# Performance work log

Hardware: AMD Instinct MI355X
Metric: run time of the kernel (lower is better)

## Reference

```python
import jax, jax.numpy as jnp
import numpy as np

N, D, H, E, TOP_K = 8192, 1024, 4096, 8, 2


def setup_inputs() -> dict:
    key = jax.random.key(0)
    ks = jax.random.split(key, 6)
    input_batch = jax.random.normal(ks[0], (N, D), dtype=jnp.float32)
    # Router-style top-k: distinct expert ids per token, softmax-normalized weights
    logits = jax.random.normal(ks[1], (N, E), dtype=jnp.float32)
    topk_vals, indices = jax.lax.top_k(logits, TOP_K)          # [N, k]
    probabilities = jax.nn.softmax(topk_vals, axis=-1)          # [N, k]
    scale1 = 1.0 / np.sqrt(D)
    scale2 = 1.0 / np.sqrt(H)
    W1 = jax.random.normal(ks[2], (E, D, H), dtype=jnp.float32) * scale1
    b1 = jnp.zeros((E, H), dtype=jnp.float32)
    W2 = jax.random.normal(ks[3], (E, H, D), dtype=jnp.float32) * scale2
    b2 = jnp.zeros((E, D), dtype=jnp.float32)
    return {
        "input_batch": input_batch,
        "probabilities": probabilities,
        "indices": indices.astype(jnp.int64),
        "W1": W1, "b1": b1, "W2": W2, "b2": b2,
    }


def reference(input_batch, probabilities, indices, W1, b1, W2, b2):
    # Each expert is Linear(D->H) + ReLU + Linear(H->D).
    # Dense per-expert forward (batched GEMM over the expert axis), then
    # gather the top_k selected expert outputs per token and combine with
    # router probabilities applied AFTER the experts:
    #   out[n] = sum_k p[n,k] * expert_{idx[n,k]}(x[n])
    h = jax.nn.relu(jnp.einsum("nd,edh->enh", input_batch, W1) + b1[:, None, :])
    y = jnp.einsum("enh,eho->eno", h, W2) + b2[:, None, :]      # [E, N, D]
    y_tok = jnp.swapaxes(y, 0, 1)                                # [N, E, D]
    sel = jnp.take_along_axis(y_tok, indices[:, :, None], axis=1)  # [N, k, D]
    output = jnp.sum(probabilities[:, :, None] * sel, axis=1)    # [N, D]
    total_loss = jnp.asarray(0.0, dtype=input_batch.dtype)       # sampler+expert losses are zero here
    return output, total_loss
```

## Files before the change

kernel.cpp:

```cpp
#include <hip/hip_runtime.h>
#include <hip/hip_bf16.h>

#define N_TOK 8192
#define DDIM 1024
#define HDIM 4096
#define NEXP 8
#define TOPK 2
#define NK (N_TOK*TOPK)
#define BM 128
#define BK 32
#define MAXT 136

typedef __hip_bfloat16 bf16;
typedef __attribute__((ext_vector_type(8))) short bf16x8;
typedef __attribute__((ext_vector_type(4))) float f32x4;

__device__ __forceinline__ void gload16(const void* g, void* lds) {
  auto l = (__attribute__((address_space(3))) unsigned int*)(unsigned int)(unsigned long long)lds;
  auto gg = (const __attribute__((address_space(1))) unsigned int*)(unsigned long long)g;
  __builtin_amdgcn_global_load_lds(gg, l, 16, 0, 0);
}

__global__ void k_router(const int* __restrict__ idx, int stride,
                         int* __restrict__ offp, int* __restrict__ texp,
                         int* __restrict__ tok, int* __restrict__ pos) {
  __shared__ int cnt[NEXP], so[NEXP + 1], off2[NEXP], scnt[NEXP];
  int tid = threadIdx.x;
  if (tid < NEXP) cnt[tid] = 0;
  __syncthreads();
  for (int r = tid; r < NK; r += blockDim.x) {
    int e = idx[r * stride];
    e = min(max(e, 0), NEXP - 1);
    atomicAdd(&cnt[e], 1);
  }
  __syncthreads();
  if (tid == 0) {
    int cum = 0;
    for (int e = 0; e < NEXP; e++) {
      so[e] = cum;
      cum += ((cnt[e] + BM - 1) / BM) * BM;
    }
    so[NEXP] = cum;
    for (int e = 0; e <= NEXP; e++) offp[e] = so[e];
  }
  __syncthreads();
  if (tid < NEXP) { off2[tid] = so[tid]; scnt[tid] = cnt[tid]; }
  __syncthreads();
  for (int r = tid; r < NK; r += blockDim.x) {
    int e = idx[r * stride];
    e = min(max(e, 0), NEXP - 1);
    int p = atomicAdd(&off2[e], 1);
    tok[p] = r >> 1;
    pos[r] = p;
  }
  int total_tiles = so[NEXP] / BM;
  for (int t = tid; t < MAXT; t += blockDim.x) {
    int e = -1;
    if (t < total_tiles) {
      for (int q = 0; q < NEXP; q++)
        if (t * BM >= so[q] && t * BM < so[q + 1]) e = q;
    }
    texp[t] = e;
  }
  for (int e = 0; e < NEXP; e++) {
    int start = so[e] + scnt[e], end = so[e + 1];
    for (int i = start + tid; i < end; i += blockDim.x) tok[i] = 0;
  }
}

__global__ void k_cvt_x(const float* __restrict__ x, bf16* __restrict__ xb) {
  int i = blockIdx.x * blockDim.x + threadIdx.x;
  if (i >= N_TOK * DDIM / 8) return;
  float4 a = ((const float4*)x)[(size_t)i * 2];
  float4 b = ((const float4*)x)[(size_t)i * 2 + 1];
  union { bf16 h[8]; uint4 v; } u;
  u.h[0] = __float2bfloat16(a.x); u.h[1] = __float2bfloat16(a.y);
  u.h[2] = __float2bfloat16(a.z); u.h[3] = __float2bfloat16(a.w);
  u.h[4] = __float2bfloat16(b.x); u.h[5] = __float2bfloat16(b.y);
  u.h[6] = __float2bfloat16(b.z); u.h[7] = __float2bfloat16(b.w);
  *(uint4*)&xb[(size_t)i * 8] = u.v;
}

__global__ void k_transpose(const float* __restrict__ in, bf16* __restrict__ out,
                            int R, int C) {
  __shared__ float t[32][65];
  size_t ebase = (size_t)blockIdx.z * R * C;
  int r0 = blockIdx.y * 32, c0 = blockIdx.x * 64;
  int tid = threadIdx.x;
  {
    int lr = tid >> 3, lc = (tid & 7) * 8;
    const float4* src = (const float4*)&in[ebase + (size_t)(r0 + lr) * C + c0 + lc];
    float4 a = src[0], b = src[1];
    t[lr][lc + 0] = a.x; t[lr][lc + 1] = a.y; t[lr][lc + 2] = a.z; t[lr][lc + 3] = a.w;
    t[lr][lc + 4] = b.x; t[lr][lc + 5] = b.y; t[lr][lc + 6] = b.z; t[lr][lc + 7] = b.w;
  }
  __syncthreads();
  {
    int sc = tid >> 2, sr = (tid & 3) * 8;
    union { bf16 h[8]; uint4 v; } u;
#pragma unroll
    for (int j = 0; j < 8; j++) u.h[j] = __float2bfloat16(t[sr + j][sc]);
    *(uint4*)&out[ebase + (size_t)(c0 + sc) * R + r0 + sr] = u.v;
  }
}

template<int MODE>
__global__ __launch_bounds__(512, 4) void k_gemm(
    const bf16* __restrict__ A, const bf16* __restrict__ Bt,
    const float* __restrict__ bias, const int* __restrict__ texp,
    const int* __restrict__ tok, int tile_base, void* __restrict__ Cout)
{
  constexpr int KT   = MODE ? HDIM : DDIM;
  constexpr int NCOL = MODE ? DDIM : HDIM;
  constexpr int BN   = 256;
  constexpr int GX   = NCOL / BN;
  constexpr int NT   = KT / BK;
  constexpr int BUFB = (BM + BN) * BK * 2;

  int nwg = gridDim.x, orig = blockIdx.x;
  int q8 = nwg >> 3, r8 = nwg & 7;
  int xcd = orig & 7, jj0 = orig >> 3;
  int w = (xcd < r8 ? xcd * (q8 + 1) : r8 * (q8 + 1) + (xcd - r8) * q8) + jj0;
  int tn = w % GX;
  int tmr = w / GX;
  int tm = tile_base + tmr;
  int e = texp[tm];
  if (e < 0) return;

  int tid = threadIdx.x, lane = tid & 63, wid = tid >> 6;
  int wm = wid >> 2, wn = wid & 3;
  int lr = lane & 15, kg = lane >> 4;

  __shared__ __align__(16) char lds[3 * BUFB];

  unsigned goff[3];
  {
    int row = tid >> 2, c = tid & 3;
    int ch = c ^ ((row >> 1) & 3);
    int arow = MODE ? (tmr * BM + row) : tok[tm * BM + row];
    goff[0] = (unsigned)(arow * KT + ch * 8);
    goff[1] = (unsigned)((e * NCOL + tn * BN + row) * KT + ch * 8);
    goff[2] = (unsigned)((e * NCOL + tn * BN + 128 + row) * KT + ch * 8);
  }

  auto stage = [&](int kt, int buf) {
    char* base = lds + buf * BUFB;
    gload16(A + goff[0] + kt * BK, base + tid * 16);
    gload16(Bt + goff[1] + kt * BK, base + 8192 + tid * 16);
    gload16(Bt + goff[2] + kt * BK, base + 16384 + tid * 16);
  };

  f32x4 acc[4][4];
#pragma unroll
  for (int i = 0; i < 4; i++)
#pragma unroll
    for (int j = 0; j < 4; j++) acc[i][j] = (f32x4){0.f, 0.f, 0.f, 0.f};

  stage(0, 0);
  stage(1, 1);
  asm volatile("s_waitcnt vmcnt(3)" ::: "memory");
  __builtin_amdgcn_s_barrier();

#pragma unroll 1
  for (int kt = 0; kt < NT; ++kt) {
    if (kt + 2 < NT) stage(kt + 2, (kt + 2) % 3);

    const char* base = lds + (kt % 3) * BUFB;
    bf16x8 av[4], bv[4];
#pragma unroll
    for (int mi = 0; mi < 4; ++mi) {
      int m = wm * 64 + mi * 16 + lr;
      int slot = kg ^ ((m >> 1) & 3);
      av[mi] = *(const bf16x8*)(base + m * 64 + slot * 16);
    }
#pragma unroll
    for (int ni = 0; ni < 4; ++ni) {
      int n = wn * 64 + ni * 16 + lr;
      int slot = kg ^ ((n >> 1) & 3);
      bv[ni] = *(const bf16x8*)(base + 8192 + n * 64 + slot * 16);
    }

#pragma unroll
    for (int mi = 0; mi < 4; ++mi)
#pragma unroll
      for (int ni = 0; ni < 4; ++ni)
        acc[mi][ni] = __builtin_amdgcn_mfma_f32_16x16x32_bf16(
            av[mi], bv[ni], acc[mi][ni], 0, 0, 0);

    if (kt + 1 < NT) {
      if (kt + 2 < NT) asm volatile("s_waitcnt vmcnt(3)" ::: "memory");
      else             asm volatile("s_waitcnt vmcnt(0)" ::: "memory");
      __builtin_amdgcn_s_barrier();
    }
  }

  const float* be = bias + (size_t)e * NCOL;
  int crow0 = (MODE ? tm : tmr) * BM;
#pragma unroll
  for (int ni = 0; ni < 4; ++ni) {
    int n = tn * BN + wn * 64 + ni * 16 + lr;
    float bvv = be[n];
#pragma unroll
    for (int mi = 0; mi < 4; ++mi) {
#pragma unroll
      for (int j = 0; j < 4; j++) {
        int mrow = wm * 64 + mi * 16 + kg * 4 + j;
        float v = acc[mi][ni][j] + bvv;
        if (MODE == 0) v = fmaxf(v, 0.f);
        ((bf16*)Cout)[(size_t)(crow0 + mrow) * NCOL + n] = __float2bfloat16(v);
      }
    }
  }
}

__global__ void k_combine(const bf16* __restrict__ y, const float* __restrict__ prob,
                          const int* __restrict__ pos, float* __restrict__ out) {
  int gid = blockIdx.x * blockDim.x + threadIdx.x;
  if (gid >= N_TOK * DDIM / 8) return;
  int n = gid >> 7;
  int d8 = gid & 127;
  int r0 = pos[2 * n], r1 = pos[2 * n + 1];
  float p0 = prob[2 * n], p1 = prob[2 * n + 1];
  uint4 a = *(const uint4*)&y[(size_t)r0 * DDIM + d8 * 8];
  uint4 b = *(const uint4*)&y[(size_t)r1 * DDIM + d8 * 8];
  const unsigned short* ah = (const unsigned short*)&a;
  const unsigned short* bh = (const unsigned short*)&b;
  float o[8];
#pragma unroll
  for (int k = 0; k < 8; k++) {
    float fa = __uint_as_float((unsigned)ah[k] << 16);
    float fb = __uint_as_float((unsigned)bh[k] << 16);
    o[k] = p0 * fa + p1 * fb;
  }
  float4* op = (float4*)&out[(size_t)n * DDIM + d8 * 8];
  op[0] = (float4){o[0], o[1], o[2], o[3]};
  op[1] = (float4){o[4], o[5], o[6], o[7]};
  if (gid == 0) out[(size_t)N_TOK * DDIM] = 0.f;
}

extern "C" void kernel_launch(void* const* d_in, const int* in_sizes, int n_in,
                              void* d_out, int out_size, void* d_ws, size_t ws_size,
                              hipStream_t stream) {
  const float* x    = (const float*)d_in[0];
  const float* prob = (const float*)d_in[1];
  const int*   idx  = (const int*)d_in[2];
  const float* W1   = (const float*)d_in[3];
  const float* b1   = (const float*)d_in[4];
  const float* W2   = (const float*)d_in[5];
  const float* b2   = (const float*)d_in[6];
  float* out = (float*)d_out;
  int stride = (in_sizes[2] == NK) ? 1 : 2;

  char* ws = (char*)d_ws;
  size_t cur = 0;
  auto alloc = [&](size_t bytes) -> void* {
    cur = (cur + 255) & ~(size_t)255;
    void* p = ws + cur; cur += bytes; return p;
  };
  int* offp  = (int*)alloc((NEXP + 1) * 4);
  int* texp  = (int*)alloc(MAXT * 4);
  int* tok   = (int*)alloc((size_t)MAXT * BM * 4);
  int* pos   = (int*)alloc((size_t)NK * 4);
  bf16* Xb   = (bf16*)alloc((size_t)N_TOK * DDIM * 2);
  bf16* W1t  = (bf16*)alloc((size_t)NEXP * HDIM * DDIM * 2);
  bf16* W2t  = (bf16*)alloc((size_t)NEXP * DDIM * HDIM * 2);
  bf16* ybuf = (bf16*)alloc((size_t)MAXT * BM * DDIM * 2);
  cur = (cur + 255) & ~(size_t)255;
  size_t h_off = cur;
  size_t h_avail = ws_size > h_off ? ws_size - h_off : 0;
  long long ts_ll = (long long)(h_avail / ((size_t)BM * HDIM * 2));
  int ts = (int)(ts_ll < 1 ? 1 : (ts_ll > MAXT ? MAXT : ts_ll));
  bf16* hbuf = (bf16*)(ws + h_off);

  k_router<<<1, 1024, 0, stream>>>(idx, stride, offp, texp, tok, pos);
  k_cvt_x<<<(N_TOK * DDIM / 8 + 255) / 256, 256, 0, stream>>>(x, Xb);
  k_transpose<<<dim3(HDIM / 64, DDIM / 32, NEXP), 256, 0, stream>>>(W1, W1t, DDIM, HDIM);
  k_transpose<<<dim3(DDIM / 64, HDIM / 32, NEXP), 256, 0, stream>>>(W2, W2t, HDIM, DDIM);

  for (int base = 0; base < MAXT; base += ts) {
    int cnt_t = (MAXT - base < ts) ? (MAXT - base) : ts;
    k_gemm<0><<<dim3(cnt_t * (HDIM / 256)), 512, 0, stream>>>(
        Xb, W1t, b1, texp, tok, base, (void*)hbuf);
    k_gemm<1><<<dim3(cnt_t * (DDIM / 256)), 512, 0, stream>>>(
        hbuf, W2t, b2, texp, tok, base, (void*)ybuf);
  }
  k_combine<<<(N_TOK * DDIM / 8 + 255) / 256, 256, 0, stream>>>(ybuf, prob, pos, out);
}
```

Measured before the change: 471.0 us.

## Enlarge GEMM tiles to 256x256x64 with 8-phase ping-pong LDS schedule

Increases the expert GEMM tile from 128x256 to 256x256 rows and the K step from 32 to 64. The main loop is restructured into an 8-phase double-buffered schedule that interleaves LDS reads, global-to-LDS loads and MFMA quarters, separated by barriers, and uses s_setprio to favour MFMA issue. The aim is higher arithmetic intensity per byte loaded and better overlap of memory with compute. The cost is lower occupancy (2 blocks per CU, 128KB LDS), more padding waste per expert tile, and a higher register footprint.

```diff
diff --git a/kernel.cpp b/kernel.cpp
--- a/kernel.cpp
+++ b/kernel.cpp
@@ -7,9 +7,9 @@
 #define NEXP 8
 #define TOPK 2
 #define NK (N_TOK*TOPK)
-#define BM 128
-#define BK 32
-#define MAXT 136
+#define BM 256
+#define BK 64
+#define MAXT 72
 
 typedef __hip_bfloat16 bf16;
 typedef __attribute__((ext_vector_type(8))) short bf16x8;
@@ -105,17 +105,17 @@
 }
 
 template<int MODE>
-__global__ __launch_bounds__(512, 4) void k_gemm(
+__global__ __launch_bounds__(512, 2) void k_gemm(
     const bf16* __restrict__ A, const bf16* __restrict__ Bt,
     const float* __restrict__ bias, const int* __restrict__ texp,
     const int* __restrict__ tok, int tile_base, void* __restrict__ Cout)
 {
-  constexpr int KT   = MODE ? HDIM : DDIM;
-  constexpr int NCOL = MODE ? DDIM : HDIM;
-  constexpr int BN   = 256;
-  constexpr int GX   = NCOL / BN;
-  constexpr int NT   = KT / BK;
-  constexpr int BUFB = (BM + BN) * BK * 2;
+  constexpr int KT    = MODE ? HDIM : DDIM;
+  constexpr int NCOL  = MODE ? DDIM : HDIM;
+  constexpr int GX    = NCOL / 256;
+  constexpr int NT    = KT / BK;
+  constexpr int NITER = NT / 2;
+  constexpr int BUFB  = 65536;
 
   int nwg = gridDim.x, orig = blockIdx.x;
   int q8 = nwg >> 3, r8 = nwg & 7;
@@ -131,86 +131,142 @@
   int wm = wid >> 2, wn = wid & 3;
   int lr = lane & 15, kg = lane >> 4;
 
-  __shared__ __align__(16) char lds[3 * BUFB];
-
-  unsigned goff[3];
-  {
-    int row = tid >> 2, c = tid & 3;
-    int ch = c ^ ((row >> 1) & 3);
-    int arow = MODE ? (tmr * BM + row) : tok[tm * BM + row];
-    goff[0] = (unsigned)(arow * KT + ch * 8);
-    goff[1] = (unsigned)((e * NCOL + tn * BN + row) * KT + ch * 8);
-    goff[2] = (unsigned)((e * NCOL + tn * BN + 128 + row) * KT + ch * 8);
-  }
-
-  auto stage = [&](int kt, int buf) {
-    char* base = lds + buf * BUFB;
-    gload16(A + goff[0] + kt * BK, base + tid * 16);
-    gload16(Bt + goff[1] + kt * BK, base + 8192 + tid * 16);
-    gload16(Bt + goff[2] + kt * BK, base + 16384 + tid * 16);
-  };
-
-  f32x4 acc[4][4];
-#pragma unroll
-  for (int i = 0; i < 4; i++)
+  __shared__ __align__(16) char lds[2 * BUFB];
+
+  unsigned aoff[2][2], boff[2][2];
+#pragma unroll
+  for (int h = 0; h < 2; ++h) {
+#pragma unroll
+    for (int it = 0; it < 2; ++it) {
+      int idx = it * 512 + tid, rl = idx >> 3, c = idx & 7;
+      int ch = c ^ (rl & 7);
+      int arow = MODE ? (tmr * BM + h * 128 + rl) : tok[tm * BM + h * 128 + rl];
+      aoff[h][it] = (unsigned)(arow * KT + ch * 8);
+      boff[h][it] = (unsigned)((e * NCOL + tn * 256 + h * 128 + rl) * KT + ch * 8);
+    }
+  }
+
+  auto stA = [&](int kt, int h) {
+    char* dst = lds + (kt & 1) * BUFB + h * 16384;
+    gload16(A + (size_t)aoff[h][0] + kt * BK, dst + tid * 16);
+    gload16(A + (size_t)aoff[h][1] + kt * BK, dst + 8192 + tid * 16);
+  };
+  auto stB = [&](int kt, int h) {
+    char* dst = lds + (kt & 1) * BUFB + 32768 + h * 16384;
+    gload16(Bt + (size_t)boff[h][0] + kt * BK, dst + tid * 16);
+    gload16(Bt + (size_t)boff[h][1] + kt * BK, dst + 8192 + tid * 16);
+  };
+
+  f32x4 acc[8][4];
+#pragma unroll
+  for (int i = 0; i < 8; i++)
 #pragma unroll
     for (int j = 0; j < 4; j++) acc[i][j] = (f32x4){0.f, 0.f, 0.f, 0.f};
 
-  stage(0, 0);
-  stage(1, 1);
-  asm volatile("s_waitcnt vmcnt(3)" ::: "memory");
-  __builtin_amdgcn_s_barrier();
+  bf16x8 bv[8];
+  auto readB8 = [&](const char* buf) {
+    const char* bb = buf + 32768;
+#pragma unroll
+    for (int ni = 0; ni < 4; ++ni)
+#pragma unroll
+      for (int kh = 0; kh < 2; ++kh) {
+        int r = wn * 64 + ni * 16 + lr;
+        int ck = (kh * 4 + kg) ^ (r & 7);
+        bv[ni * 2 + kh] = *(const bf16x8*)(bb + r * 128 + ck * 16);
+      }
+  };
+  auto readA4 = [&](const char* buf, int q, bf16x8* av) {
+#pragma unroll
+    for (int g = 0; g < 2; ++g)
+#pragma unroll
+      for (int kh = 0; kh < 2; ++kh) {
+        int r = wm * 128 + (q * 2 + g) * 16 + lr;
+        int ck = (kh * 4 + kg) ^ (r & 7);
+        av[g * 2 + kh] = *(const bf16x8*)(buf + r * 128 + ck * 16);
+      }
+  };
+  auto mfmaQ = [&](int q, bf16x8* av) {
+    __builtin_amdgcn_s_setprio(1);
+#pragma unroll
+    for (int g = 0; g < 2; ++g)
+#pragma unroll
+      for (int ni = 0; ni < 4; ++ni)
+#pragma unroll
+        for (int kh = 0; kh < 2; ++kh)
+          acc[q * 2 + g][ni] = __builtin_amdgcn_mfma_f32_16x16x32_bf16(
+              av[g * 2 + kh], bv[ni * 2 + kh], acc[q * 2 + g][ni], 0, 0, 0);
+    __builtin_amdgcn_s_setprio(0);
+  };
+
+#define BAR()    __builtin_amdgcn_s_barrier()
+#define LGKM0()  asm volatile("s_waitcnt lgkmcnt(0)" ::: "memory")
+#define LGKM8()  asm volatile("s_waitcnt lgkmcnt(8)" ::: "memory")
+
+  stA(0, 0); stA(0, 1); stB(0, 0); stB(0, 1);
+  stB(1, 0); stB(1, 1);
+  asm volatile("s_waitcnt vmcnt(4)" ::: "memory");
+  BAR();
+
+  const char* b0 = lds;
+  const char* b1 = lds + BUFB;
 
 #pragma unroll 1
-  for (int kt = 0; kt < NT; ++kt) {
-    if (kt + 2 < NT) stage(kt + 2, (kt + 2) % 3);
-
-    const char* base = lds + (kt % 3) * BUFB;
-    bf16x8 av[4], bv[4];
-#pragma unroll
-    for (int mi = 0; mi < 4; ++mi) {
-      int m = wm * 64 + mi * 16 + lr;
-      int slot = kg ^ ((m >> 1) & 3);
-      av[mi] = *(const bf16x8*)(base + m * 64 + slot * 16);
-    }
-#pragma unroll
-    for (int ni = 0; ni < 4; ++ni) {
-      int n = wn * 64 + ni * 16 + lr;
-      int slot = kg ^ ((n >> 1) & 3);
-      bv[ni] = *(const bf16x8*)(base + 8192 + n * 64 + slot * 16);
-    }
-
-#pragma unroll
-    for (int mi = 0; mi < 4; ++mi)
-#pragma unroll
-      for (int ni = 0; ni < 4; ++ni)
-        acc[mi][ni] = __builtin_amdgcn_mfma_f32_16x16x32_bf16(
-            av[mi], bv[ni], acc[mi][ni], 0, 0, 0);
-
-    if (kt + 1 < NT) {
-      if (kt + 2 < NT) asm volatile("s_waitcnt vmcnt(3)" ::: "memory");
-      else             asm volatile("s_waitcnt vmcnt(0)" ::: "memory");
-      __builtin_amdgcn_s_barrier();
-    }
+  for (int i = 0; i < NITER; ++i) {
+    int t = 2 * i;
+    bool last = (i == NITER - 1);
+    bf16x8 av[4];
+
+    readB8(b0); readA4(b0, 0, av);
+    stA(t + 1, 0);
+    LGKM8();
+    BAR(); LGKM0(); mfmaQ(0, av); BAR();
+
+    readA4(b0, 1, av); stA(t + 1, 1);
+    BAR(); LGKM0(); mfmaQ(1, av); BAR();
+
+    readA4(b0, 2, av); if (!last) stB(t + 2, 0);
+    BAR(); LGKM0(); mfmaQ(2, av); BAR();
+
+    readA4(b0, 3, av); if (!last) stB(t + 2, 1);
+    if (last) { asm volatile("s_waitcnt vmcnt(0)" ::: "memory"); }
+    else      { asm volatile("s_waitcnt vmcnt(4)" ::: "memory"); }
+    BAR(); LGKM0(); mfmaQ(3, av); BAR();
+
+    readB8(b1); readA4(b1, 0, av); if (!last) stA(t + 2, 0);
+    LGKM8();
+    BAR(); LGKM0(); mfmaQ(0, av); BAR();
+
+    readA4(b1, 1, av); if (!last) stA(t + 2, 1);
+    BAR(); LGKM0(); mfmaQ(1, av); BAR();
+
+    readA4(b1, 2, av); if (!last) stB(t + 3, 0);
+    BAR(); LGKM0(); mfmaQ(2, av); BAR();
+
+    readA4(b1, 3, av); if (!last) stB(t + 3, 1);
+    if (!last) { asm volatile("s_waitcnt vmcnt(4)" ::: "memory"); }
+    BAR(); LGKM0(); mfmaQ(3, av); BAR();
   }
 
   const float* be = bias + (size_t)e * NCOL;
   int crow0 = (MODE ? tm : tmr) * BM;
 #pragma unroll
   for (int ni = 0; ni < 4; ++ni) {
-    int n = tn * BN + wn * 64 + ni * 16 + lr;
+    int n = tn * 256 + wn * 64 + ni * 16 + lr;
     float bvv = be[n];
 #pragma unroll
-    for (int mi = 0; mi < 4; ++mi) {
+    for (int mi = 0; mi < 8; ++mi) {
 #pragma unroll
       for (int j = 0; j < 4; j++) {
-        int mrow = wm * 64 + mi * 16 + kg * 4 + j;
+        int mrow = wm * 128 + mi * 16 + kg * 4 + j;
         float v = acc[mi][ni][j] + bvv;
         if (MODE == 0) v = fmaxf(v, 0.f);
         ((bf16*)Cout)[(size_t)(crow0 + mrow) * NCOL + n] = __float2bfloat16(v);
       }
     }
   }
+#undef BAR
+#undef LGKM0
+#undef LGKM8
 }
 
 __global__ void k_combine(const bf16* __restrict__ y, const float* __restrict__ prob,
```

Measured after the change: 489.5 us. 1.04x slower.
